# Kernel optimization log

Hardware: AMD Instinct MI355X
Metric: run time of the kernel (lower is better)

## Reference

```python
import jax, jax.numpy as jnp
import numpy as np

HDIM = 4
P = 2 ** HDIM  # 16 hypercube nodes


def build_dense_weight(hweight, out_features, in_features):
    # hweight: [hdim+1, P, ob, ib]; assemble dense [out_features, in_features]
    ob = out_features // P
    ib = in_features // P
    i = jnp.arange(P)
    w = jnp.zeros((P, P, ob, ib), dtype=hweight.dtype)
    # diagonal blocks: w[i, i] = hweight[0, i]
    w = w.at[i, i].set(hweight[0])
    # hypercube neighbor blocks: w[i ^ (1<<d), i] = hweight[d+1, i]
    for d in range(HDIM):
        j = i ^ (1 << d)
        w = w.at[j, i].set(hweight[d + 1])
    # permute (0,2,1,3) then reshape -> [out_features, in_features]
    w = jnp.transpose(w, (0, 2, 1, 3)).reshape(out_features, in_features)
    return w


def setup_inputs() -> dict:
    key = jax.random.key(0)
    k1, k2, k3 = jax.random.split(key, 3)
    in_features, out_features = 4096, 4096
    ob = out_features // P
    ib = in_features // P
    x = jax.random.normal(k1, (8192, in_features), dtype=jnp.float32)
    # kaiming-uniform-like scale for the block weights
    bound_w = 1.0 / np.sqrt(ib)
    hweight = jax.random.uniform(k2, (HDIM + 1, P, ob, ib), dtype=jnp.float32,
                                 minval=-bound_w, maxval=bound_w)
    bound_b = 1.0 / np.sqrt(in_features * (HDIM + 1))
    hbias = jax.random.uniform(k3, (out_features,), dtype=jnp.float32,
                               minval=-bound_b, maxval=bound_b)
    return {"x": x, "hweight": hweight, "hbias": hbias}


def reference(x, hweight, hbias):
    out_features = hweight.shape[1] * hweight.shape[2]
    in_features = hweight.shape[1] * hweight.shape[3]
    w = build_dense_weight(hweight, out_features, in_features)
    # F.linear(x, w, b) = x @ w.T + b
    return x @ w.T + hbias
```

## Files before the change

kernel.cpp:

```cpp
#include <hip/hip_runtime.h>

typedef __attribute__((ext_vector_type(8))) short short8;
typedef __attribute__((ext_vector_type(4))) float f32x4;

#define INF 4096
#define NKT 40
#define BUFB 32768

#define AS1 __attribute__((address_space(1)))
#define AS3 __attribute__((address_space(3)))

__device__ __forceinline__ unsigned short f2bf(float f) {
    unsigned int u = __float_as_uint(f);
    u += 0x7FFFu + ((u >> 16) & 1u);
    return (unsigned short)(u >> 16);
}

__device__ __forceinline__ void gl_lds16(const unsigned short* g, void* l) {
    __builtin_amdgcn_global_load_lds((const AS1 void*)g, (AS3 void*)l, 16, 0, 0);
}

__device__ __forceinline__ int swz(int b) { return b ^ ((b >> 3) & 0x30); }

__global__ __launch_bounds__(256)
void cvt_bf16(const float* __restrict__ x, const float* __restrict__ hw,
              unsigned short* __restrict__ xb, unsigned short* __restrict__ wb)
{
    const long long NX = 8192LL * 4096;
    const long long NW = 5LL * 16 * 256 * 256;
    const long long total8 = (NX + NW) / 8;
    for (long long i = (long long)blockIdx.x * 256 + threadIdx.x; i < total8;
         i += (long long)gridDim.x * 256) {
        long long e = i * 8;
        const float* src;
        unsigned short* dst;
        long long off;
        if (e < NX) { src = x;  dst = xb; off = e; }
        else        { src = hw; dst = wb; off = e - NX; }
        float4 f0 = *(const float4*)(src + off);
        float4 f1 = *(const float4*)(src + off + 4);
        ushort4 u0, u1;
        u0.x = f2bf(f0.x); u0.y = f2bf(f0.y); u0.z = f2bf(f0.z); u0.w = f2bf(f0.w);
        u1.x = f2bf(f1.x); u1.y = f2bf(f1.y); u1.z = f2bf(f1.z); u1.w = f2bf(f1.w);
        *(ushort4*)(dst + off)     = u0;
        *(ushort4*)(dst + off + 4) = u1;
    }
}

__global__ __launch_bounds__(512, 2)
void hcl_gemm8(const unsigned short* __restrict__ xb,
               const unsigned short* __restrict__ wb,
               const float* __restrict__ hb,
               float* __restrict__ out)
{
    extern __shared__ unsigned short lds[];

    const int tid  = threadIdx.x;
    const int lane = tid & 63;
    const int wave = tid >> 6;
    const int wr   = wave >> 2;
    const int wcn  = wave & 3;
    const int ln15 = lane & 15;
    const int hi   = lane >> 4;

    const int bm0 = blockIdx.x * 256;
    const int p   = blockIdx.y;

    const int b0 = tid * 16;
    const int b1 = (512 + tid) * 16;
    const int g0 = swz(b0), g1 = swz(b1);
    const int rS0 = g0 >> 6, cS0 = (g0 & 63) >> 1;
    const int rS1 = g1 >> 6, cS1 = (g1 & 63) >> 1;

    int offA[8], offB[4];
    #pragma unroll
    for (int mf = 0; mf < 8; ++mf) {
        int row = wr * 128 + mf * 16 + ln15;
        offA[mf] = swz(row * 64 + hi * 16);
    }
    #pragma unroll
    for (int nf = 0; nf < 4; ++nf) {
        int row = wcn * 64 + nf * 16 + ln15;
        offB[nf] = swz(row * 64 + hi * 16);
    }

    f32x4 acc[8][4] = {};

    auto STAGE = [&](int kt, int buf) {
        const int t = kt >> 3;
        const int s = p ^ ((1 << t) >> 1);
        const unsigned short* ga = xb + (size_t)bm0 * INF + s * 256 + (kt & 7) * 32;
        const unsigned short* gb = wb + ((size_t)(t * 16 + s) << 16) + (kt & 7) * 32;
        char* lb = (char*)lds + buf * BUFB + wave * 1024;
        gl_lds16(ga + (size_t)rS0 * INF + cS0, lb);
        gl_lds16(ga + (size_t)rS1 * INF + cS1, lb + 8192);
        gl_lds16(gb + (size_t)rS0 * 256 + cS0, lb + 16384);
        gl_lds16(gb + (size_t)rS1 * 256 + cS1, lb + 16384 + 8192);
    };

    auto COMPUTE = [&](int buf) {
        const char* LA = (const char*)lds + buf * BUFB;
        const char* LB = LA + 16384;
        short8 fa[8], fb[4];
        #pragma unroll
        for (int nf = 0; nf < 4; ++nf) fb[nf] = *(const short8*)(LB + offB[nf]);
        #pragma unroll
        for (int mf = 0; mf < 8; ++mf) fa[mf] = *(const short8*)(LA + offA[mf]);
        __builtin_amdgcn_s_setprio(1);
        #pragma unroll
        for (int mf = 0; mf < 8; ++mf)
            #pragma unroll
            for (int nf = 0; nf < 4; ++nf)
                acc[mf][nf] = __builtin_amdgcn_mfma_f32_16x16x32_bf16(
                    fa[mf], fb[nf], acc[mf][nf], 0, 0, 0);
        __builtin_amdgcn_s_setprio(0);
    };

    STAGE(0, 0);
    STAGE(1, 1);

    for (int kt = 0; kt < NKT - 2; ++kt) {
        STAGE(kt + 2, (kt + 2) % 3);
        asm volatile("s_waitcnt vmcnt(8)");
        __builtin_amdgcn_s_barrier();
        __builtin_amdgcn_sched_barrier(0);
        COMPUTE(kt % 3);
        __builtin_amdgcn_s_barrier();
        __builtin_amdgcn_sched_barrier(0);
    }
    asm volatile("s_waitcnt vmcnt(4)");
    __builtin_amdgcn_s_barrier();
    __builtin_amdgcn_sched_barrier(0);
    COMPUTE((NKT - 2) % 3);
    __builtin_amdgcn_s_barrier();
    asm volatile("s_waitcnt vmcnt(0)");
    __builtin_amdgcn_s_barrier();
    __builtin_amdgcn_sched_barrier(0);
    COMPUTE((NKT - 1) % 3);

    const int col0 = p * 256 + wcn * 64;
    #pragma unroll
    for (int nf = 0; nf < 4; ++nf) {
        const int col = col0 + nf * 16 + ln15;
        const float bias = hb[col];
        #pragma unroll
        for (int mf = 0; mf < 8; ++mf) {
            #pragma unroll
            for (int r = 0; r < 4; ++r) {
                const int row = bm0 + wr * 128 + mf * 16 + hi * 4 + r;
                out[(size_t)row * 4096 + col] = acc[mf][nf][r] + bias;
            }
        }
    }
}

__global__ __launch_bounds__(256)
void hcl_mfma_fused(const float* __restrict__ x,
                    const float* __restrict__ hw,
                    const float* __restrict__ hb,
                    float* __restrict__ out)
{
    __shared__ unsigned short As[128][32];
    __shared__ unsigned short Bs[128][32];

    const int tid  = threadIdx.x;
    const int lane = tid & 63;
    const int wave = tid >> 6;
    const int wr   = wave >> 1, wc = wave & 1;

    const int bm0 = blockIdx.x * 128;
    const int p   = blockIdx.y >> 1;
    const int nh  = blockIdx.y & 1;

    f32x4 acc[4][4] = {};

    const int srow = tid >> 3;
    const int scol = (tid & 7) * 4;

    #pragma unroll
    for (int t = 0; t < 5; ++t) {
        const int mask = (t == 0) ? 0 : (1 << (t - 1));
        const int s = p ^ mask;
        const float* xchunk = x  + (size_t)bm0 * INF + s * 256;
        const float* wchunk = hw + ((size_t)(t * 16 + s) * 256 + nh * 128) * 256;

        for (int k8 = 0; k8 < 8; ++k8) {
            const int kc = k8 * 32;
            #pragma unroll
            for (int i = 0; i < 4; ++i) {
                const int row = i * 32 + srow;
                float4 fa = *(const float4*)(xchunk + (size_t)row * INF + kc + scol);
                float4 fb = *(const float4*)(wchunk + (size_t)row * 256 + kc + scol);
                ushort4 ua, ub;
                ua.x = f2bf(fa.x); ua.y = f2bf(fa.y);
                ua.z = f2bf(fa.z); ua.w = f2bf(fa.w);
                ub.x = f2bf(fb.x); ub.y = f2bf(fb.y);
                ub.z = f2bf(fb.z); ub.w = f2bf(fb.w);
                *(ushort4*)&As[row][scol] = ua;
                *(ushort4*)&Bs[row][scol] = ub;
            }
            __syncthreads();

            short8 a[4], b[4];
            #pragma unroll
            for (int mi = 0; mi < 4; ++mi)
                a[mi] = *(const short8*)&As[wr * 64 + mi * 16 + (lane & 15)][(lane >> 4) * 8];
            #pragma unroll
            for (int nj = 0; nj < 4; ++nj)
                b[nj] = *(const short8*)&Bs[wc * 64 + nj * 16 + (lane & 15)][(lane >> 4) * 8];

            #pragma unroll
            for (int mi = 0; mi < 4; ++mi)
                #pragma unroll
                for (int nj = 0; nj < 4; ++nj)
                    acc[mi][nj] = __builtin_amdgcn_mfma_f32_16x16x32_bf16(
                        a[mi], b[nj], acc[mi][nj], 0, 0, 0);

            __syncthreads();
        }
    }

    const int col0 = p * 256 + nh * 128 + wc * 64;
    #pragma unroll
    for (int nj = 0; nj < 4; ++nj) {
        const int col = col0 + nj * 16 + (lane & 15);
        const float bias = hb[col];
        #pragma unroll
        for (int mi = 0; mi < 4; ++mi) {
            #pragma unroll
            for (int r = 0; r < 4; ++r) {
                const int row = bm0 + wr * 64 + mi * 16 + (lane >> 4) * 4 + r;
                out[(size_t)row * 4096 + col] = acc[mi][nj][r] + bias;
            }
        }
    }
}

extern "C" void kernel_launch(void* const* d_in, const int* in_sizes, int n_in,
                              void* d_out, int out_size, void* d_ws, size_t ws_size,
                              hipStream_t stream) {
    const float* x  = (const float*)d_in[0];
    const float* hw = (const float*)d_in[1];
    const float* hb = (const float*)d_in[2];
    float* out = (float*)d_out;

    const size_t NX = 8192ull * 4096;
    const size_t NW = 5ull * 16 * 256 * 256;
    const size_t need = (NX + NW) * sizeof(unsigned short);

    if (ws_size >= need) {
        unsigned short* xb = (unsigned short*)d_ws;
        unsigned short* wb = xb + NX;
        cvt_bf16<<<2048, 256, 0, stream>>>(x, hw, xb, wb);
        dim3 grid(8192 / 256, 16);
        hcl_gemm8<<<grid, 512, 3 * BUFB, stream>>>(xb, wb, hb, out);
    } else {
        dim3 grid(8192 / 128, 32);
        hcl_mfma_fused<<<grid, 256, 0, stream>>>(x, hw, hb, out);
    }
}
```

Before: 154.4 us.

## Shrink GEMM block tile to 128x256 with four waves per block

```diff
diff --git a/kernel.cpp b/kernel.cpp
--- a/kernel.cpp
+++ b/kernel.cpp
@@ -5,7 +5,7 @@
 
 #define INF 4096
 #define NKT 40
-#define BUFB 32768
+#define BUFB 24576
 
 #define AS1 __attribute__((address_space(1)))
 #define AS3 __attribute__((address_space(3)))
@@ -47,8 +47,8 @@
     }
 }
 
-__global__ __launch_bounds__(512, 2)
-void hcl_gemm8(const unsigned short* __restrict__ xb,
+__global__ __launch_bounds__(256, 2)
+void hcl_gemm4(const unsigned short* __restrict__ xb,
                const unsigned short* __restrict__ wb,
                const float* __restrict__ hb,
                float* __restrict__ out)
@@ -58,31 +58,27 @@
     const int tid  = threadIdx.x;
     const int lane = tid & 63;
     const int wave = tid >> 6;
-    const int wr   = wave >> 2;
-    const int wcn  = wave & 3;
     const int ln15 = lane & 15;
     const int hi   = lane >> 4;
 
-    const int bm0 = blockIdx.x * 256;
+    const int bm0 = blockIdx.x * 128;
     const int p   = blockIdx.y;
 
-    const int b0 = tid * 16;
-    const int b1 = (512 + tid) * 16;
-    const int g0 = swz(b0), g1 = swz(b1);
-    const int rS0 = g0 >> 6, cS0 = (g0 & 63) >> 1;
-    const int rS1 = g1 >> 6, cS1 = (g1 & 63) >> 1;
+    int rj[4], cj[4];
+    #pragma unroll
+    for (int j = 0; j < 4; ++j) {
+        int g = swz(j * 4096 + tid * 16);
+        rj[j] = g >> 6;
+        cj[j] = (g & 63) >> 1;
+    }
 
     int offA[8], offB[4];
     #pragma unroll
-    for (int mf = 0; mf < 8; ++mf) {
-        int row = wr * 128 + mf * 16 + ln15;
-        offA[mf] = swz(row * 64 + hi * 16);
-    }
-    #pragma unroll
-    for (int nf = 0; nf < 4; ++nf) {
-        int row = wcn * 64 + nf * 16 + ln15;
-        offB[nf] = swz(row * 64 + hi * 16);
-    }
+    for (int mf = 0; mf < 8; ++mf)
+        offA[mf] = swz((mf * 16 + ln15) * 64 + hi * 16);
+    #pragma unroll
+    for (int nf = 0; nf < 4; ++nf)
+        offB[nf] = swz((wave * 64 + nf * 16 + ln15) * 64 + hi * 16);
 
     f32x4 acc[8][4] = {};
 
@@ -92,15 +88,17 @@
         const unsigned short* ga = xb + (size_t)bm0 * INF + s * 256 + (kt & 7) * 32;
         const unsigned short* gb = wb + ((size_t)(t * 16 + s) << 16) + (kt & 7) * 32;
         char* lb = (char*)lds + buf * BUFB + wave * 1024;
-        gl_lds16(ga + (size_t)rS0 * INF + cS0, lb);
-        gl_lds16(ga + (size_t)rS1 * INF + cS1, lb + 8192);
-        gl_lds16(gb + (size_t)rS0 * 256 + cS0, lb + 16384);
-        gl_lds16(gb + (size_t)rS1 * 256 + cS1, lb + 16384 + 8192);
+        gl_lds16(ga + (size_t)rj[0] * INF + cj[0], lb);
+        gl_lds16(ga + (size_t)rj[1] * INF + cj[1], lb + 4096);
+        gl_lds16(gb + (size_t)rj[0] * 256 + cj[0], lb + 8192);
+        gl_lds16(gb + (size_t)rj[1] * 256 + cj[1], lb + 8192 + 4096);
+        gl_lds16(gb + (size_t)rj[2] * 256 + cj[2], lb + 8192 + 8192);
+        gl_lds16(gb + (size_t)rj[3] * 256 + cj[3], lb + 8192 + 12288);
     };
 
     auto COMPUTE = [&](int buf) {
         const char* LA = (const char*)lds + buf * BUFB;
-        const char* LB = LA + 16384;
+        const char* LB = LA + 8192;
         short8 fa[8], fb[4];
         #pragma unroll
         for (int nf = 0; nf < 4; ++nf) fb[nf] = *(const short8*)(LB + offB[nf]);
@@ -121,14 +119,14 @@
 
     for (int kt = 0; kt < NKT - 2; ++kt) {
         STAGE(kt + 2, (kt + 2) % 3);
-        asm volatile("s_waitcnt vmcnt(8)");
+        asm volatile("s_waitcnt vmcnt(12)");
         __builtin_amdgcn_s_barrier();
         __builtin_amdgcn_sched_barrier(0);
         COMPUTE(kt % 3);
         __builtin_amdgcn_s_barrier();
         __builtin_amdgcn_sched_barrier(0);
     }
-    asm volatile("s_waitcnt vmcnt(4)");
+    asm volatile("s_waitcnt vmcnt(6)");
     __builtin_amdgcn_s_barrier();
     __builtin_amdgcn_sched_barrier(0);
     COMPUTE((NKT - 2) % 3);
@@ -138,7 +136,7 @@
     __builtin_amdgcn_sched_barrier(0);
     COMPUTE((NKT - 1) % 3);
 
-    const int col0 = p * 256 + wcn * 64;
+    const int col0 = p * 256 + wave * 64;
     #pragma unroll
     for (int nf = 0; nf < 4; ++nf) {
         const int col = col0 + nf * 16 + ln15;
@@ -147,7 +145,7 @@
         for (int mf = 0; mf < 8; ++mf) {
             #pragma unroll
             for (int r = 0; r < 4; ++r) {
-                const int row = bm0 + wr * 128 + mf * 16 + hi * 4 + r;
+                const int row = bm0 + mf * 16 + hi * 4 + r;
                 out[(size_t)row * 4096 + col] = acc[mf][nf][r] + bias;
             }
         }
@@ -252,8 +250,8 @@
         unsigned short* xb = (unsigned short*)d_ws;
         unsigned short* wb = xb + NX;
         cvt_bf16<<<2048, 256, 0, stream>>>(x, hw, xb, wb);
-        dim3 grid(8192 / 256, 16);
-        hcl_gemm8<<<grid, 512, 3 * BUFB, stream>>>(xb, wb, hb, out);
+        dim3 grid(8192 / 128, 16);
+        hcl_gemm4<<<grid, 256, 3 * BUFB, stream>>>(xb, wb, hb, out);
     } else {
         dim3 grid(8192 / 128, 32);
         hcl_mfma_fused<<<grid, 256, 0, stream>>>(x, hw, hb, out);
```

Result: no change. 155.0 us (+0.4%).
